# Optimization experiments

Measured on AMD Instinct MI355X. Metric: run time of the kernel, lower is better.

## Reference

```python
import jax, jax.numpy as jnp
import numpy as np

H = 1024           # hidden_size
E = 8              # num_experts
I = 4096 // E      # expert_intermediate_size = 512
V = 32000          # vocab_size
T = 4096           # num_tokens


def setup_inputs() -> dict:
    key = jax.random.key(0)
    ks = jax.random.split(key, 6)
    x = jax.random.normal(ks[0], (T, H), dtype=jnp.float32)
    token_ids = jax.random.randint(ks[1], (T,), 0, V, dtype=jnp.int64)
    mu = jax.random.normal(ks[2], (T, H), dtype=jnp.float32)
    # learned parameters (kaiming-like scale)
    gate_up_proj = jax.random.normal(ks[3], (E, H, 2 * I), dtype=jnp.float32) * (1.0 / np.sqrt(H))
    down_proj = jax.random.normal(ks[4], (E, I, H), dtype=jnp.float32) * (1.0 / np.sqrt(I))
    mu_w = jax.random.normal(ks[5], (E, H), dtype=jnp.float32) * 0.02  # mu_router.weight [E, H]
    return {"x": x, "token_ids": token_ids, "mu": mu,
            "gate_up_proj": gate_up_proj, "down_proj": down_proj, "mu_w": mu_w}


def reference(x, token_ids, mu, gate_up_proj, down_proj, mu_w):
    # deterministic base routing: expert = token_id % num_experts
    tid = jnp.clip(token_ids, 0, V - 1)
    base_expert = tid % E                                   # [T]
    # mu router biases the routing decision
    mu_logits = mu @ mu_w.T                                 # [T, E]
    combined = jax.nn.one_hot(base_expert, E, dtype=jnp.float32) * 10.0 + mu_logits
    expert_ids = jnp.argmax(combined, axis=-1)              # [T]

    out = jnp.zeros_like(x)
    # fixed small loop over experts; rows not routed to e are discarded by the mask,
    # so computing the dense GEMM over all tokens gives identical selected rows.
    for e in range(E):
        mask = (expert_ids == e)                            # [T]
        gu = x @ gate_up_proj[e]                            # [T, 2I]
        gate, up = gu[:, :I], gu[:, I:]
        inter = jax.nn.silu(gate) * up                      # [T, I]
        y = inter @ down_proj[e]                            # [T, H]
        out = jnp.where(mask[:, None], y, out)
    return out
```

## Files before the change

### kernel.cpp

```cpp
#include <hip/hip_runtime.h>
#include <cmath>

constexpr int T_DIM = 4096;
constexpr int H_DIM = 1024;
constexpr int E_DIM = 8;
constexpr int I_DIM = 512;
constexpr int V_DIM = 32000;

typedef _Float16 half_t;
typedef __attribute__((ext_vector_type(8))) _Float16 halfx8;
typedef __attribute__((ext_vector_type(4))) _Float16 halfx4;
typedef __attribute__((ext_vector_type(4))) float floatx4;

#define GLOAD16(g, l)                                                        \
    __builtin_amdgcn_global_load_lds(                                        \
        (const __attribute__((address_space(1))) void*)(g),                  \
        (__attribute__((address_space(3))) void*)(l), 16, 0, 0)

constexpr size_t OFF_COUNTS = 0;
constexpr size_t OFF_EID    = 1024;
constexpr size_t OFF_TOKL   = OFF_EID + (size_t)T_DIM * 4;
constexpr size_t OFF_XB     = OFF_TOKL + (size_t)E_DIM * T_DIM * 4;
constexpr size_t OFF_GUPT   = OFF_XB + (size_t)T_DIM * H_DIM * 2;
constexpr size_t OFF_DOWNT  = OFF_GUPT + (size_t)E_DIM * 2 * I_DIM * H_DIM * 2;
constexpr size_t OFF_INTER  = OFF_DOWNT + (size_t)E_DIM * H_DIM * I_DIM * 2;

__global__ __launch_bounds__(256) void prep_all_kernel(
    const float* __restrict__ x, const float* __restrict__ gup,
    const float* __restrict__ down, const float* __restrict__ mu,
    const int* __restrict__ token_ids, const float* __restrict__ mu_w,
    half_t* __restrict__ xb, half_t* __restrict__ gupT,
    half_t* __restrict__ downT, int* __restrict__ expert_id)
{
    const int z = blockIdx.z, tid = threadIdx.x;

    if (z >= 17) {
        const int t = (z - 17) * 256 + blockIdx.y * 16 + blockIdx.x;

        const float4 m = *(const float4*)&mu[(size_t)t * H_DIM + tid * 4];
        float acc[E_DIM];
#pragma unroll
        for (int e = 0; e < E_DIM; ++e) {
            const float4 w = *(const float4*)&mu_w[e * H_DIM + tid * 4];
            acc[e] = m.x * w.x + m.y * w.y + m.z * w.z + m.w * w.w;
        }
#pragma unroll
        for (int e = 0; e < E_DIM; ++e) {
#pragma unroll
            for (int off = 32; off > 0; off >>= 1)
                acc[e] += __shfl_down(acc[e], off, 64);
        }
        __shared__ float part[4][E_DIM];
        const int lane = tid & 63, w = tid >> 6;
        if (lane == 0) {
#pragma unroll
            for (int e = 0; e < E_DIM; ++e) part[w][e] = acc[e];
        }
        __syncthreads();
        if (tid == 0) {
            int tk = token_ids[t];
            tk = min(max(tk, 0), V_DIM - 1);
            const int be = tk & (E_DIM - 1);
            float best = -1e30f; int bi = 0;
#pragma unroll
            for (int e = 0; e < E_DIM; ++e) {
                const float c = part[0][e] + part[1][e] + part[2][e] + part[3][e]
                              + (e == be ? 10.f : 0.f);
                if (c > best) { best = c; bi = e; }
            }
            expert_id[t] = bi;
        }
        return;
    }

    if (z == 16) {
        const int blk = blockIdx.y * 16 + blockIdx.x;
#pragma unroll
        for (int p = 0; p < 16; ++p) {
            const size_t i = (size_t)blk * 16384 + p * 1024 + tid * 4;
            const float4 v = *(const float4*)&x[i];
            halfx4 h = { (half_t)v.x, (half_t)v.y, (half_t)v.z, (half_t)v.w };
            *(halfx4*)&xb[i] = h;
        }
        return;
    }

    __shared__ float tile[64][65];
    const float* se;  half_t* de;  int K;
    if (z < 8) {
        se = gup + (size_t)z * H_DIM * (2 * I_DIM);
        de = gupT + (size_t)z * (2 * I_DIM) * H_DIM;
        K = H_DIM;
    } else {
        if (blockIdx.y >= 8) return;
        const int e = z - 8;
        se = down + (size_t)e * I_DIM * H_DIM;
        de = downT + (size_t)e * H_DIM * I_DIM;
        K = I_DIM;
    }
    constexpr int N = 1024;
    const int n0 = blockIdx.x * 64, k0 = blockIdx.y * 64;
    const int c4 = (tid & 15) * 4, r0 = tid >> 4;
#pragma unroll
    for (int p = 0; p < 4; ++p) {
        const int r = r0 + p * 16;
        const float4 v = *(const float4*)&se[(size_t)(k0 + r) * N + n0 + c4];
        tile[r][c4 + 0] = v.x; tile[r][c4 + 1] = v.y;
        tile[r][c4 + 2] = v.z; tile[r][c4 + 3] = v.w;
    }
    __syncthreads();
#pragma unroll
    for (int p = 0; p < 4; ++p) {
        const int n = r0 + p * 16;
        const int kc = (tid & 15) * 4;
        halfx4 h = { (half_t)tile[kc + 0][n], (half_t)tile[kc + 1][n],
                     (half_t)tile[kc + 2][n], (half_t)tile[kc + 3][n] };
        *(halfx4*)&de[(size_t)(n0 + n) * K + k0 + kc] = h;
    }
}

__global__ __launch_bounds__(256) void scatter_kernel(
    const int* __restrict__ expert_id, int* __restrict__ counts,
    int* __restrict__ tok_list)
{
    const int tid = threadIdx.x;
    __shared__ int cnt[E_DIM];
    if (tid < E_DIM) cnt[tid] = 0;
    __syncthreads();
    for (int i = tid; i < T_DIM; i += 256) {
        const int e = expert_id[i];
        const int pos = atomicAdd(&cnt[e], 1);
        tok_list[e * T_DIM + pos] = i;
    }
    __syncthreads();
    if (tid < E_DIM) counts[tid] = cnt[tid];
}

__global__ __launch_bounds__(256) void gemm1_mfma_kernel(
    const half_t* __restrict__ xb, const half_t* __restrict__ gupT,
    const int* __restrict__ counts, const int* __restrict__ tok_list,
    half_t* __restrict__ inter)
{
    const int e = blockIdx.x;
    const int count = counts[e];
    const int m0 = blockIdx.z * 64;
    if (m0 >= count) return;
    const int n0 = blockIdx.y * 64;

    __shared__ __align__(16) half_t As[64 * 64];
    __shared__ __align__(16) half_t Bs[128 * 64];
    __shared__ int toks[64];

    const int tid = threadIdx.x;
    if (tid < 64) {
        const int m = m0 + tid;
        toks[tid] = (m < count) ? tok_list[e * T_DIM + m] : -1;
    }
    __syncthreads();

    const half_t* We = gupT + (size_t)e * (2 * I_DIM) * H_DIM;

    const int lane = tid & 63;
    const int w = tid >> 6;
    const int lr = lane >> 3, lc = lane & 7;

    const half_t* aptr[2]; const half_t* bptr[4];
    half_t *alds[2], *blds[4];
#pragma unroll
    for (int j = 0; j < 2; ++j) {
        const int r = w * 16 + j * 8 + lr;
        const int cg = lc ^ (r & 7);
        const int tk = toks[r];
        aptr[j] = xb + (size_t)(tk < 0 ? 0 : tk) * H_DIM + cg * 8;
        alds[j] = &As[(w * 16 + j * 8) * 64];
    }
#pragma unroll
    for (int j = 0; j < 4; ++j) {
        const int n = w * 32 + j * 8 + lr;
        const int col = (n < 64) ? (n0 + n) : (I_DIM + n0 + (n - 64));
        const int cg = lc ^ (n & 7);
        bptr[j] = We + (size_t)col * H_DIM + cg * 8;
        blds[j] = &Bs[(w * 32 + j * 8) * 64];
    }

    const floatx4 fzero = {0.f, 0.f, 0.f, 0.f};
    floatx4 accg[2][2], accu[2][2];
#pragma unroll
    for (int i = 0; i < 2; ++i)
#pragma unroll
        for (int j = 0; j < 2; ++j) { accg[i][j] = fzero; accu[i][j] = fzero; }

    const int wr = w >> 1, wc = w & 1;
    const int fm = lane & 15, q = lane >> 4;
    const int fm7 = fm & 7;

    for (int k0 = 0; k0 < H_DIM; k0 += 64) {
#pragma unroll
        for (int j = 0; j < 2; ++j) GLOAD16(aptr[j] + k0, alds[j]);
#pragma unroll
        for (int j = 0; j < 4; ++j) GLOAD16(bptr[j] + k0, blds[j]);
        __syncthreads();

#pragma unroll
        for (int ks = 0; ks < 2; ++ks) {
            const int swz = ((ks * 4 + q) ^ fm7) * 8;
            const halfx8 a0 = *(const halfx8*)&As[(32 * wr + fm) * 64 + swz];
            const halfx8 a1 = *(const halfx8*)&As[(32 * wr + 16 + fm) * 64 + swz];
#pragma unroll
            for (int ct = 0; ct < 2; ++ct) {
                const int ng = wc * 32 + ct * 16 + fm;
                const halfx8 bg = *(const halfx8*)&Bs[ng * 64 + swz];
                const halfx8 bu = *(const halfx8*)&Bs[(64 + ng) * 64 + swz];
                accg[0][ct] = __builtin_amdgcn_mfma_f32_16x16x32_f16(a0, bg, accg[0][ct], 0, 0, 0);
                accg[1][ct] = __builtin_amdgcn_mfma_f32_16x16x32_f16(a1, bg, accg[1][ct], 0, 0, 0);
                accu[0][ct] = __builtin_amdgcn_mfma_f32_16x16x32_f16(a0, bu, accu[0][ct], 0, 0, 0);
                accu[1][ct] = __builtin_amdgcn_mfma_f32_16x16x32_f16(a1, bu, accu[1][ct], 0, 0, 0);
            }
        }
        __syncthreads();
    }

#pragma unroll
    for (int rt = 0; rt < 2; ++rt)
#pragma unroll
        for (int r = 0; r < 4; ++r) {
            const int row = 32 * wr + 16 * rt + q * 4 + r;
            const int tk = toks[row];
            if (tk < 0) continue;
#pragma unroll
            for (int ct = 0; ct < 2; ++ct) {
                const float g = accg[rt][ct][r];
                const float u = accu[rt][ct][r];
                const float s = g / (1.f + __expf(-g)) * u;
                inter[(size_t)tk * I_DIM + n0 + wc * 32 + ct * 16 + fm] = (half_t)s;
            }
        }
}

__global__ __launch_bounds__(256) void gemm2_mfma_kernel(
    const half_t* __restrict__ inter, const half_t* __restrict__ downT,
    const int* __restrict__ counts, const int* __restrict__ tok_list,
    float* __restrict__ out)
{
    const int e = blockIdx.x;
    const int count = counts[e];
    const int m0 = blockIdx.z * 64;
    if (m0 >= count) return;
    const int n0 = blockIdx.y * 128;

    __shared__ __align__(16) half_t As[64 * 64];
    __shared__ __align__(16) half_t Bs[128 * 64];
    __shared__ int toks[64];

    const int tid = threadIdx.x;
    if (tid < 64) {
        const int m = m0 + tid;
        toks[tid] = (m < count) ? tok_list[e * T_DIM + m] : -1;
    }
    __syncthreads();

    const half_t* De = downT + (size_t)e * H_DIM * I_DIM;

    const int lane = tid & 63;
    const int w = tid >> 6;
    const int lr = lane >> 3, lc = lane & 7;

    const half_t* aptr[2]; const half_t* bptr[4];
    half_t *alds[2], *blds[4];
#pragma unroll
    for (int j = 0; j < 2; ++j) {
        const int r = w * 16 + j * 8 + lr;
        const int cg = lc ^ (r & 7);
        const int tk = toks[r];
        aptr[j] = inter + (size_t)(tk < 0 ? 0 : tk) * I_DIM + cg * 8;
        alds[j] = &As[(w * 16 + j * 8) * 64];
    }
#pragma unroll
    for (int j = 0; j < 4; ++j) {
        const int n = w * 32 + j * 8 + lr;
        const int cg = lc ^ (n & 7);
        bptr[j] = De + (size_t)(n0 + n) * I_DIM + cg * 8;
        blds[j] = &Bs[(w * 32 + j * 8) * 64];
    }

    const floatx4 fzero = {0.f, 0.f, 0.f, 0.f};
    floatx4 acc[2][4];
#pragma unroll
    for (int i = 0; i < 2; ++i)
#pragma unroll
        for (int j = 0; j < 4; ++j) acc[i][j] = fzero;

    const int wr = w >> 1, wc = w & 1;
    const int fm = lane & 15, q = lane >> 4;
    const int fm7 = fm & 7;

    for (int k0 = 0; k0 < I_DIM; k0 += 64) {
#pragma unroll
        for (int j = 0; j < 2; ++j) GLOAD16(aptr[j] + k0, alds[j]);
#pragma unroll
        for (int j = 0; j < 4; ++j) GLOAD16(bptr[j] + k0, blds[j]);
        __syncthreads();

#pragma unroll
        for (int ks = 0; ks < 2; ++ks) {
            const int swz = ((ks * 4 + q) ^ fm7) * 8;
            const halfx8 a0 = *(const halfx8*)&As[(32 * wr + fm) * 64 + swz];
            const halfx8 a1 = *(const halfx8*)&As[(32 * wr + 16 + fm) * 64 + swz];
#pragma unroll
            for (int ct = 0; ct < 4; ++ct) {
                const halfx8 b = *(const halfx8*)&Bs[(wc * 64 + ct * 16 + fm) * 64 + swz];
                acc[0][ct] = __builtin_amdgcn_mfma_f32_16x16x32_f16(a0, b, acc[0][ct], 0, 0, 0);
                acc[1][ct] = __builtin_amdgcn_mfma_f32_16x16x32_f16(a1, b, acc[1][ct], 0, 0, 0);
            }
        }
        __syncthreads();
    }

#pragma unroll
    for (int rt = 0; rt < 2; ++rt)
#pragma unroll
        for (int r = 0; r < 4; ++r) {
            const int row = 32 * wr + 16 * rt + q * 4 + r;
            const int tk = toks[row];
            if (tk < 0) continue;
#pragma unroll
            for (int ct = 0; ct < 4; ++ct)
                out[(size_t)tk * H_DIM + n0 + wc * 64 + ct * 16 + fm] = acc[rt][ct][r];
        }
}

extern "C" void kernel_launch(void* const* d_in, const int* in_sizes, int n_in,
                              void* d_out, int out_size, void* d_ws, size_t ws_size,
                              hipStream_t stream)
{
    const float* x         = (const float*)d_in[0];
    const int*   token_ids = (const int*)  d_in[1];
    const float* mu        = (const float*)d_in[2];
    const float* gup       = (const float*)d_in[3];
    const float* down      = (const float*)d_in[4];
    const float* mu_w      = (const float*)d_in[5];
    float* out = (float*)d_out;

    char* ws = (char*)d_ws;
    int*    counts    = (int*)(ws + OFF_COUNTS);
    int*    expert_id = (int*)(ws + OFF_EID);
    int*    tok_list  = (int*)(ws + OFF_TOKL);
    half_t* xb        = (half_t*)(ws + OFF_XB);
    half_t* gupT      = (half_t*)(ws + OFF_GUPT);
    half_t* downT     = (half_t*)(ws + OFF_DOWNT);
    half_t* inter     = (half_t*)(ws + OFF_INTER);

    prep_all_kernel<<<dim3(16, 16, 33), 256, 0, stream>>>(
        x, gup, down, mu, token_ids, mu_w, xb, gupT, downT, expert_id);
    scatter_kernel<<<1, 256, 0, stream>>>(expert_id, counts, tok_list);
    gemm1_mfma_kernel<<<dim3(E_DIM, 8, T_DIM / 64), 256, 0, stream>>>(
        xb, gupT, counts, tok_list, inter);
    gemm2_mfma_kernel<<<dim3(E_DIM, 8, T_DIM / 64), 256, 0, stream>>>(
        inter, downT, counts, tok_list, out);
}
```

Before: 159.5 us.

## Fuse routing scatter into prep kernel and move down_proj transpose into gemm1

```diff
diff --git a/kernel.cpp b/kernel.cpp
--- a/kernel.cpp
+++ b/kernel.cpp
@@ -17,6 +17,7 @@
         (const __attribute__((address_space(1))) void*)(g),                  \
         (__attribute__((address_space(3))) void*)(l), 16, 0, 0)
 
+constexpr int  CNT_STRIDE  = 16;
 constexpr size_t OFF_COUNTS = 0;
 constexpr size_t OFF_EID    = 1024;
 constexpr size_t OFF_TOKL   = OFF_EID + (size_t)T_DIM * 4;
@@ -25,55 +26,73 @@
 constexpr size_t OFF_DOWNT  = OFF_GUPT + (size_t)E_DIM * 2 * I_DIM * H_DIM * 2;
 constexpr size_t OFF_INTER  = OFF_DOWNT + (size_t)E_DIM * H_DIM * I_DIM * 2;
 
-__global__ __launch_bounds__(256) void prep_all_kernel(
+__global__ __launch_bounds__(256) void prep_kernel(
     const float* __restrict__ x, const float* __restrict__ gup,
-    const float* __restrict__ down, const float* __restrict__ mu,
-    const int* __restrict__ token_ids, const float* __restrict__ mu_w,
-    half_t* __restrict__ xb, half_t* __restrict__ gupT,
-    half_t* __restrict__ downT, int* __restrict__ expert_id)
+    const float* __restrict__ mu, const int* __restrict__ token_ids,
+    const float* __restrict__ mu_w, half_t* __restrict__ xb,
+    half_t* __restrict__ gupT, int* __restrict__ counts,
+    int* __restrict__ tok_list)
 {
     const int z = blockIdx.z, tid = threadIdx.x;
 
-    if (z >= 17) {
-        const int t = (z - 17) * 256 + blockIdx.y * 16 + blockIdx.x;
-
-        const float4 m = *(const float4*)&mu[(size_t)t * H_DIM + tid * 4];
+    if (z == 0) {
+        const int blk = blockIdx.y * 16 + blockIdx.x;
+        if (blk >= T_DIM / 64) return;
+        const int j = tid >> 2;
+        const int q = tid & 3;
+        const int t = blk * 64 + j;
+
         float acc[E_DIM];
 #pragma unroll
+        for (int e = 0; e < E_DIM; ++e) acc[e] = 0.f;
+        const float4* mrow  = (const float4*)&mu[(size_t)t * H_DIM + q * 256];
+        const float4* wbase = (const float4*)&mu_w[q * 256];
+        for (int i = 0; i < 64; ++i) {
+            const float4 m = mrow[i];
+#pragma unroll
+            for (int e = 0; e < E_DIM; ++e) {
+                const float4 w = wbase[(size_t)e * (H_DIM / 4) + i];
+                acc[e] += m.x * w.x + m.y * w.y + m.z * w.z + m.w * w.w;
+            }
+        }
+#pragma unroll
         for (int e = 0; e < E_DIM; ++e) {
-            const float4 w = *(const float4*)&mu_w[e * H_DIM + tid * 4];
-            acc[e] = m.x * w.x + m.y * w.y + m.z * w.z + m.w * w.w;
-        }
-#pragma unroll
-        for (int e = 0; e < E_DIM; ++e) {
-#pragma unroll
-            for (int off = 32; off > 0; off >>= 1)
-                acc[e] += __shfl_down(acc[e], off, 64);
-        }
-        __shared__ float part[4][E_DIM];
-        const int lane = tid & 63, w = tid >> 6;
-        if (lane == 0) {
-#pragma unroll
-            for (int e = 0; e < E_DIM; ++e) part[w][e] = acc[e];
-        }
-        __syncthreads();
-        if (tid == 0) {
+            acc[e] += __shfl_down(acc[e], 1, 64);
+            acc[e] += __shfl_down(acc[e], 2, 64);
+        }
+        __shared__ int eid[64];
+        if (q == 0) {
             int tk = token_ids[t];
             tk = min(max(tk, 0), V_DIM - 1);
             const int be = tk & (E_DIM - 1);
             float best = -1e30f; int bi = 0;
 #pragma unroll
             for (int e = 0; e < E_DIM; ++e) {
-                const float c = part[0][e] + part[1][e] + part[2][e] + part[3][e]
-                              + (e == be ? 10.f : 0.f);
+                const float c = acc[e] + (e == be ? 10.f : 0.f);
                 if (c > best) { best = c; bi = e; }
             }
-            expert_id[t] = bi;
+            eid[j] = bi;
+        }
+        __syncthreads();
+        if (tid < 64) {
+            const int mye = eid[tid];
+            for (int e = 0; e < E_DIM; ++e) {
+                const unsigned long long mask = __ballot(mye == e);
+                if (mye == e) {
+                    const int leader = __builtin_ctzll(mask);
+                    const int rank = (int)__popcll(mask & ((1ull << tid) - 1ull));
+                    int base = 0;
+                    if (tid == leader)
+                        base = atomicAdd(&counts[e * CNT_STRIDE], (int)__popcll(mask));
+                    base = __shfl(base, leader, 64);
+                    tok_list[e * T_DIM + base + rank] = blk * 64 + tid;
+                }
+            }
         }
         return;
     }
 
-    if (z == 16) {
+    if (z == 9) {
         const int blk = blockIdx.y * 16 + blockIdx.x;
 #pragma unroll
         for (int p = 0; p < 16; ++p) {
@@ -86,19 +105,10 @@
     }
 
     __shared__ float tile[64][65];
-    const float* se;  half_t* de;  int K;
-    if (z < 8) {
-        se = gup + (size_t)z * H_DIM * (2 * I_DIM);
-        de = gupT + (size_t)z * (2 * I_DIM) * H_DIM;
-        K = H_DIM;
-    } else {
-        if (blockIdx.y >= 8) return;
-        const int e = z - 8;
-        se = down + (size_t)e * I_DIM * H_DIM;
-        de = downT + (size_t)e * H_DIM * I_DIM;
-        K = I_DIM;
-    }
-    constexpr int N = 1024;
+    const int e = z - 1;
+    const float* se = gup + (size_t)e * H_DIM * (2 * I_DIM);
+    half_t* de = gupT + (size_t)e * (2 * I_DIM) * H_DIM;
+    constexpr int N = 1024, K = H_DIM;
     const int n0 = blockIdx.x * 64, k0 = blockIdx.y * 64;
     const int c4 = (tid & 15) * 4, r0 = tid >> 4;
 #pragma unroll
@@ -112,46 +122,57 @@
 #pragma unroll
     for (int p = 0; p < 4; ++p) {
         const int n = r0 + p * 16;
-        const int kc = (tid & 15) * 4;
+        const int kc = c4;
         halfx4 h = { (half_t)tile[kc + 0][n], (half_t)tile[kc + 1][n],
                      (half_t)tile[kc + 2][n], (half_t)tile[kc + 3][n] };
         *(halfx4*)&de[(size_t)(n0 + n) * K + k0 + kc] = h;
     }
 }
 
-__global__ __launch_bounds__(256) void scatter_kernel(
-    const int* __restrict__ expert_id, int* __restrict__ counts,
-    int* __restrict__ tok_list)
-{
-    const int tid = threadIdx.x;
-    __shared__ int cnt[E_DIM];
-    if (tid < E_DIM) cnt[tid] = 0;
-    __syncthreads();
-    for (int i = tid; i < T_DIM; i += 256) {
-        const int e = expert_id[i];
-        const int pos = atomicAdd(&cnt[e], 1);
-        tok_list[e * T_DIM + pos] = i;
-    }
-    __syncthreads();
-    if (tid < E_DIM) counts[tid] = cnt[tid];
-}
-
 __global__ __launch_bounds__(256) void gemm1_mfma_kernel(
     const half_t* __restrict__ xb, const half_t* __restrict__ gupT,
+    const float* __restrict__ down, half_t* __restrict__ downT,
     const int* __restrict__ counts, const int* __restrict__ tok_list,
     half_t* __restrict__ inter)
 {
+    __shared__ __align__(16) char smraw[64 * 64 * 2 + 128 * 64 * 2 + 64 * 4];
+    const int tid = threadIdx.x;
     const int e = blockIdx.x;
-    const int count = counts[e];
+
+    if (blockIdx.z >= 64) {
+        float (*tile)[65] = (float (*)[65])smraw;
+        const float* se = down + (size_t)e * I_DIM * H_DIM;
+        half_t* de = downT + (size_t)e * H_DIM * I_DIM;
+        const int n0 = (blockIdx.z - 64) * 64, k0 = blockIdx.y * 64;
+        const int c4 = (tid & 15) * 4, r0 = tid >> 4;
+#pragma unroll
+        for (int p = 0; p < 4; ++p) {
+            const int r = r0 + p * 16;
+            const float4 v = *(const float4*)&se[(size_t)(k0 + r) * H_DIM + n0 + c4];
+            tile[r][c4 + 0] = v.x; tile[r][c4 + 1] = v.y;
+            tile[r][c4 + 2] = v.z; tile[r][c4 + 3] = v.w;
+        }
+        __syncthreads();
+#pragma unroll
+        for (int p = 0; p < 4; ++p) {
+            const int n = r0 + p * 16;
+            const int kc = c4;
+            halfx4 h = { (half_t)tile[kc + 0][n], (half_t)tile[kc + 1][n],
+                         (half_t)tile[kc + 2][n], (half_t)tile[kc + 3][n] };
+            *(halfx4*)&de[(size_t)(n0 + n) * I_DIM + k0 + kc] = h;
+        }
+        return;
+    }
+
+    const int count = counts[e * CNT_STRIDE];
     const int m0 = blockIdx.z * 64;
     if (m0 >= count) return;
     const int n0 = blockIdx.y * 64;
 
-    __shared__ __align__(16) half_t As[64 * 64];
-    __shared__ __align__(16) half_t Bs[128 * 64];
-    __shared__ int toks[64];
-
-    const int tid = threadIdx.x;
+    half_t* const As = (half_t*)smraw;
+    half_t* const Bs = (half_t*)(smraw + 64 * 64 * 2);
+    int* const toks = (int*)(smraw + 64 * 64 * 2 + 128 * 64 * 2);
+
     if (tid < 64) {
         const int m = m0 + tid;
         toks[tid] = (m < count) ? tok_list[e * T_DIM + m] : -1;
@@ -243,7 +264,7 @@
     float* __restrict__ out)
 {
     const int e = blockIdx.x;
-    const int count = counts[e];
+    const int count = counts[e * CNT_STRIDE];
     const int m0 = blockIdx.z * 64;
     if (m0 >= count) return;
     const int n0 = blockIdx.y * 128;
@@ -343,18 +364,18 @@
 
     char* ws = (char*)d_ws;
     int*    counts    = (int*)(ws + OFF_COUNTS);
-    int*    expert_id = (int*)(ws + OFF_EID);
     int*    tok_list  = (int*)(ws + OFF_TOKL);
     half_t* xb        = (half_t*)(ws + OFF_XB);
     half_t* gupT      = (half_t*)(ws + OFF_GUPT);
     half_t* downT     = (half_t*)(ws + OFF_DOWNT);
     half_t* inter     = (half_t*)(ws + OFF_INTER);
 
-    prep_all_kernel<<<dim3(16, 16, 33), 256, 0, stream>>>(
-        x, gup, down, mu, token_ids, mu_w, xb, gupT, downT, expert_id);
-    scatter_kernel<<<1, 256, 0, stream>>>(expert_id, counts, tok_list);
-    gemm1_mfma_kernel<<<dim3(E_DIM, 8, T_DIM / 64), 256, 0, stream>>>(
-        xb, gupT, counts, tok_list, inter);
+    hipMemsetAsync(counts, 0, E_DIM * CNT_STRIDE * sizeof(int), stream);
+
+    prep_kernel<<<dim3(16, 16, 10), 256, 0, stream>>>(
+        x, gup, mu, token_ids, mu_w, xb, gupT, counts, tok_list);
+    gemm1_mfma_kernel<<<dim3(E_DIM, 8, 80), 256, 0, stream>>>(
+        xb, gupT, down, downT, counts, tok_list, inter);
     gemm2_mfma_kernel<<<dim3(E_DIM, 8, T_DIM / 64), 256, 0, stream>>>(
         inter, downT, counts, tok_list, out);
 }
```

After: 212.7 us. 1.33x slower.
